# Kernel tuning notes

Hardware: AMD Instinct MI355X
Metric: run time of the kernel (lower is better)

## Reference

```python
import jax, jax.numpy as jnp
import numpy as np


def setup_inputs() -> dict:
    key = jax.random.key(0)
    k1, k2, k3, k4, k5 = jax.random.split(key, 5)
    B, S, D, F, E = 4, 4096, 1024, 2048, 8
    top_k = 2
    num_tokens = B * S
    capacity = max(int(num_tokens / E * 1.25), 4)  # 2560
    scale = 0.02
    return {
        "x": jax.random.normal(k1, (B, S, D), dtype=jnp.float32),
        "gate_w": jax.random.normal(k2, (D, E), dtype=jnp.float32) * scale,
        "w_gate": jax.random.normal(k3, (E, D, F), dtype=jnp.float32) * scale,
        "w_up": jax.random.normal(k4, (E, D, F), dtype=jnp.float32) * scale,
        "w_down": jax.random.normal(k5, (E, F, D), dtype=jnp.float32) * scale,
        "num_experts": E,
        "top_k": top_k,
        "capacity": capacity,
    }


AUX_LOSS_WEIGHT = 0.01


def reference(x, gate_w, w_gate, w_up, w_down, num_experts, top_k, capacity):
    B, S, D = x.shape
    N = B * S
    x_flat = x.reshape(N, D)

    # ---- Router ----
    logits = x_flat @ gate_w                      # [N, E]
    probs = jax.nn.softmax(logits, axis=-1)
    weights, indices = jax.lax.top_k(probs, top_k)  # [N, K]
    weights = weights / jnp.sum(weights, axis=-1, keepdims=True)

    # ---- Capacity-based dispatch ----
    indices_flat = indices.reshape(-1)            # [N*K]
    x_rep = jnp.repeat(x_flat, top_k, axis=0)     # [N*K, D]
    expert_mask = jax.nn.one_hot(indices_flat, num_experts, dtype=jnp.int32)  # [N*K, E]
    token_priority = jnp.cumsum(expert_mask, axis=0) * expert_mask
    token_rank = jnp.sum(token_priority, axis=1)  # [N*K], 1-based rank within expert
    valid = (token_rank > 0) & (token_rank <= capacity)
    gather_idx = indices_flat * capacity + (token_rank - 1)  # [N*K]

    total_slots = num_experts * capacity
    # drop-mode scatter: invalid rows are sent out-of-bounds and dropped
    safe_idx = jnp.where(valid, gather_idx, total_slots)
    dispatched = jnp.zeros((total_slots, D), dtype=x.dtype)
    dispatched = dispatched.at[safe_idx].set(x_rep, mode="drop")
    dispatched = dispatched.reshape(num_experts, capacity, D)  # [E, C, D]

    # ---- Fused experts (grouped BMM, SwiGLU) ----
    gate = jnp.einsum("ecd,edf->ecf", dispatched, w_gate)
    up = jnp.einsum("ecd,edf->ecf", dispatched, w_up)
    hidden = jax.nn.silu(gate) * up
    expert_out = jnp.einsum("ecf,efd->ecd", hidden, w_down)
    expert_out_flat = expert_out.reshape(total_slots, D)

    # ---- Combine (row-aligned gather; dropped tokens contribute zero) ----
    gathered = expert_out_flat[jnp.clip(gather_idx, 0, total_slots - 1)]
    combined = jnp.where(valid[:, None], gathered, jnp.zeros((), dtype=x.dtype))
    combined = combined.reshape(N, top_k, D)
    output = jnp.sum(combined * weights[:, :, None], axis=1)  # [N, D]

    # ---- Aux load-balance loss ----
    mask = jax.nn.one_hot(indices, num_experts, dtype=jnp.float32).sum(axis=1)  # [N, E]
    f = mask.sum(axis=0) / (N * top_k + 1e-9)
    P = probs.mean(axis=0)
    aux_loss = num_experts * jnp.sum(f * P) * AUX_LOSS_WEIGHT

    return output.reshape(B, S, D), aux_loss
```

## Files before the change

kernel.cpp:

```cpp
#include <hip/hip_runtime.h>
#include <stdint.h>

#define N_TOK 16384
#define DIM   1024
#define NEXP  8
#define FF    2048
#define CAP   2560
#define NSLOT (NEXP*CAP)

using f32x4  = __attribute__((ext_vector_type(4))) float;
using bf16x8 = __attribute__((ext_vector_type(8))) short;

__device__ __forceinline__ unsigned short f2bf(float f){
  union { float f; unsigned u; } c; c.f = f;
  unsigned u = c.u + 0x7FFFu + ((c.u >> 16) & 1u);
  return (unsigned short)(u >> 16);
}
__device__ __forceinline__ float bf2f(unsigned short h){
  union { unsigned u; float f; } c; c.u = ((unsigned)h) << 16; return c.f;
}

__device__ __forceinline__ void gld16(const unsigned short* g, unsigned short* l){
  __builtin_amdgcn_global_load_lds((__attribute__((address_space(1))) void*)(void*)g,
                                   (__attribute__((address_space(3))) void*)l,
                                   16, 0, 0);
}

#define HBAR __builtin_amdgcn_s_barrier()

__global__ __launch_bounds__(256) void k_router(
    const float* __restrict__ x, const float* __restrict__ gate_w,
    float* __restrict__ probs, int* __restrict__ topidx, float* __restrict__ topw)
{
  __shared__ float gwT[NEXP][DIM];
  int tid = threadIdx.x;
  for (int i = tid; i < DIM*NEXP; i += 256) gwT[i & 7][i >> 3] = gate_w[i];
  __syncthreads();
  int wave = tid >> 6, lane = tid & 63;
  int t = blockIdx.x * 4 + wave;
  const float* xr = x + (size_t)t * DIM;
  double acc[NEXP];
  #pragma unroll
  for (int e = 0; e < NEXP; e++) acc[e] = 0.0;
  for (int j = 0; j < DIM/64; j++){
    double xv = (double)xr[lane + 64*j];
    #pragma unroll
    for (int e = 0; e < NEXP; e++) acc[e] += xv * (double)gwT[e][lane + 64*j];
  }
  #pragma unroll
  for (int off = 32; off >= 1; off >>= 1){
    #pragma unroll
    for (int e = 0; e < NEXP; e++) acc[e] += __shfl_xor(acc[e], off, 64);
  }
  if (lane == 0){
    double m = acc[0];
    #pragma unroll
    for (int e = 1; e < NEXP; e++) m = fmax(m, acc[e]);
    double p[NEXP], Z = 0.0;
    #pragma unroll
    for (int e = 0; e < NEXP; e++){ p[e] = exp(acc[e] - m); Z += p[e]; }
    double invZ = 1.0 / Z;
    #pragma unroll
    for (int e = 0; e < NEXP; e++){ p[e] *= invZ; probs[t*NEXP + e] = (float)p[e]; }
    int i0 = 0; double p0 = p[0];
    #pragma unroll
    for (int e = 1; e < NEXP; e++) if (p[e] > p0){ p0 = p[e]; i0 = e; }
    int i1 = (i0 == 0) ? 1 : 0; double p1 = p[i1];
    #pragma unroll
    for (int e = 0; e < NEXP; e++) if (e != i0 && p[e] > p1){ p1 = p[e]; i1 = e; }
    double s = p0 + p1;
    topidx[t*2+0] = i0; topidx[t*2+1] = i1;
    topw [t*2+0] = (float)(p0/s); topw[t*2+1] = (float)(p1/s);
  }
}

__global__ __launch_bounds__(1024) void k_scan(
    const int* __restrict__ topidx,
    int* __restrict__ slot_token, int* __restrict__ tok_slots,
    int* __restrict__ counts_total)
{
  __shared__ int sc[1024][NEXP];
  const int t = threadIdx.x;
  const int base_i = t * 32;
  int ids[32];
  #pragma unroll
  for (int j = 0; j < 32; j++) ids[j] = topidx[base_i + j];
  int b[NEXP];
  #pragma unroll
  for (int e = 0; e < NEXP; e++) b[e] = 0;
  #pragma unroll
  for (int j = 0; j < 32; j++){
    #pragma unroll
    for (int e = 0; e < NEXP; e++) if (ids[j] == e) b[e]++;
  }
  #pragma unroll
  for (int e = 0; e < NEXP; e++) sc[t][e] = b[e];
  __syncthreads();
  for (int off = 1; off < 1024; off <<= 1){
    int tmp[NEXP];
    #pragma unroll
    for (int e = 0; e < NEXP; e++) tmp[e] = (t >= off) ? sc[t-off][e] : 0;
    __syncthreads();
    #pragma unroll
    for (int e = 0; e < NEXP; e++) sc[t][e] += tmp[e];
    __syncthreads();
  }
  int myb[NEXP];
  #pragma unroll
  for (int e = 0; e < NEXP; e++) myb[e] = sc[t][e] - b[e];
  if (t == 1023){
    #pragma unroll
    for (int e = 0; e < NEXP; e++) counts_total[e] = sc[1023][e];
  }
  #pragma unroll
  for (int j = 0; j < 32; j++){
    int slot = -1;
    #pragma unroll
    for (int e = 0; e < NEXP; e++){
      if (ids[j] == e){
        int r = myb[e]; myb[e] = r + 1;
        if (r < CAP){
          slot = e*CAP + r;
          slot_token[slot] = (base_i + j) >> 1;
        }
      }
    }
    tok_slots[base_i + j] = slot;
  }
}

template<int MODE>
__global__ __launch_bounds__(256) void k_tcv(
    const float* __restrict__ in, unsigned short* __restrict__ out,
    int R, int C, size_t estride)
{
  __shared__ float tt[64][65];
  const int e  = blockIdx.z;
  const float* ine = in + (size_t)e * R * C;
  unsigned short* oute = out + (size_t)e * estride;
  const int c0 = blockIdx.x * 64, r0 = blockIdx.y * 64;
  const int tid = threadIdx.x;
  #pragma unroll
  for (int i = 0; i < 4; i++){
    int idx = i*256 + tid;
    int row = idx >> 4, c4 = idx & 15;
    float4 v = *(const float4*)(ine + (size_t)(r0 + row)*C + c0 + c4*4);
    tt[c4*4+0][row] = v.x; tt[c4*4+1][row] = v.y;
    tt[c4*4+2][row] = v.z; tt[c4*4+3][row] = v.w;
  }
  __syncthreads();
  #pragma unroll
  for (int i = 0; i < 2; i++){
    int cl = i*32 + (tid >> 3);
    int rs = (tid & 7) * 8;
    int c  = c0 + cl;
    int orow = (MODE == 0) ? ((c>>4)*32 + (c&15))
             : (MODE == 1) ? ((c>>4)*32 + 16 + (c&15))
             : c;
    unsigned long long pk0 = 0, pk1 = 0;
    #pragma unroll
    for (int j = 0; j < 4; j++) pk0 |= (unsigned long long)f2bf(tt[cl][rs+j]) << (16*j);
    #pragma unroll
    for (int j = 0; j < 4; j++) pk1 |= (unsigned long long)f2bf(tt[cl][rs+4+j]) << (16*j);
    unsigned long long* dst = (unsigned long long*)(oute + (size_t)orow*R + r0 + rs);
    dst[0] = pk0; dst[1] = pk1;
  }
}

__global__ __launch_bounds__(256) void k_gather(
    const float* __restrict__ x, const int* __restrict__ slot_token,
    unsigned short* __restrict__ disp)
{
  const int s = blockIdx.x;
  const int t = slot_token[s];
  const int tid = threadIdx.x;
  unsigned long long pk = 0ull;
  if (t >= 0){
    float4 v = *(const float4*)(x + (size_t)t*DIM + tid*4);
    pk =  (unsigned long long)f2bf(v.x)
       | ((unsigned long long)f2bf(v.y) << 16)
       | ((unsigned long long)f2bf(v.z) << 32)
       | ((unsigned long long)f2bf(v.w) << 48);
  }
  *(unsigned long long*)(disp + (size_t)s*DIM + tid*4) = pk;
}

__device__ __forceinline__ void stg(const unsigned short* gsrc, int ldg,
                                    unsigned short* Lh, int wave, int lane){
  const int sl = (lane & 3) ^ ((lane >> 3) & 3);
  #pragma unroll
  for (int j = 0; j < 2; j++){
    int bi = wave*2 + j;
    gld16(gsrc + (size_t)(bi*16 + (lane >> 2))*ldg + sl*8, Lh + bi*512);
  }
}
__device__ __forceinline__ bf16x8 frd(const unsigned short* Lh, int r, int g){
  return *(const bf16x8*)(Lh + r*32 + (((g ^ ((r >> 1) & 3))) << 3));
}
template<int MG>
__device__ __forceinline__ void mm16(f32x4 (&acc)[8][4], const bf16x8 (&a)[4], const bf16x8 (&b)[4]){
  #pragma unroll
  for (int i = 0; i < 4; i++)
    #pragma unroll
    for (int n = 0; n < 4; n++)
      acc[MG*4+i][n] = __builtin_amdgcn_mfma_f32_16x16x32_bf16(a[i], b[n], acc[MG*4+i][n], 0, 0, 0);
}

__global__ __launch_bounds__(512, 2) void k_gemm1(
    const unsigned short* __restrict__ A,
    const unsigned short* __restrict__ B,
    unsigned short* __restrict__ Out)
{
  constexpr int KDIM = DIM, NH = DIM/32;
  __shared__ unsigned short lds[65536];
  const int id = blockIdx.x;
  const int e  = id & 7;
  const int t  = id >> 3;
  const int mt = t % 10, nt = t / 10;
  const int m0 = mt*256, n0 = nt*256;
  const unsigned short* Ab = A + ((size_t)e*CAP  + m0) * KDIM;
  const unsigned short* Bb = B + ((size_t)e*2*FF + n0) * KDIM;
  const int tid = threadIdx.x, wave = tid >> 6, lane = tid & 63;
  const int wr = wave >> 2, wc = wave & 3;
  const int g = lane >> 4, l15 = lane & 15;

  f32x4 acc[8][4];
  const f32x4 z4 = {0.f,0.f,0.f,0.f};
  #pragma unroll
  for (int i = 0; i < 8; i++)
    #pragma unroll
    for (int n = 0; n < 4; n++) acc[i][n] = z4;

  stg(Ab,      KDIM, lds + 0*16384,        wave, lane);
  stg(Bb,      KDIM, lds + 0*16384 + 8192, wave, lane);
  stg(Ab + 32, KDIM, lds + 1*16384,        wave, lane);
  stg(Bb + 32, KDIM, lds + 1*16384 + 8192, wave, lane);
  stg(Ab + 64, KDIM, lds + 2*16384,        wave, lane);
  stg(Bb + 64, KDIM, lds + 2*16384 + 8192, wave, lane);

  for (int h = 0; h < NH; ++h){
    if (h < NH-2)      { asm volatile("s_waitcnt vmcnt(8)" ::: "memory"); }
    else if (h == NH-2){ asm volatile("s_waitcnt vmcnt(4)" ::: "memory"); }
    else               { asm volatile("s_waitcnt vmcnt(0)" ::: "memory"); }
    HBAR;
    __builtin_amdgcn_sched_barrier(0);
    unsigned short* LA = lds + (h & 3)*16384;
    unsigned short* LB = LA + 8192;
    if (h + 3 < NH){
      unsigned short* NS = lds + ((h+3) & 3)*16384;
      stg(Ab + (size_t)(h+3)*32, KDIM, NS,        wave, lane);
      stg(Bb + (size_t)(h+3)*32, KDIM, NS + 8192, wave, lane);
    }
    bf16x8 a[4], b[4], a2[4];
    #pragma unroll
    for (int i = 0; i < 4; i++) a[i]  = frd(LA, wr*128 + i*16 + l15, g);
    #pragma unroll
    for (int n = 0; n < 4; n++) b[n]  = frd(LB, wc*64 + n*16 + l15, g);
    #pragma unroll
    for (int i = 0; i < 4; i++) a2[i] = frd(LA, wr*128 + (4+i)*16 + l15, g);
    __builtin_amdgcn_s_setprio(1);
    mm16<0>(acc, a, b);
    mm16<1>(acc, a2, b);
    __builtin_amdgcn_s_setprio(0);
  }

  unsigned short* H = Out + ((size_t)e*CAP + m0 + wr*128) * (size_t)FF;
  const int hc0 = (n0 + wc*64) >> 1;
  #pragma unroll
  for (int mf = 0; mf < 8; mf++)
    #pragma unroll
    for (int q = 0; q < 4; q++){
      int r = mf*16 + g*4 + q;
      #pragma unroll
      for (int p = 0; p < 2; p++){
        float gg = acc[mf][2*p][q], uu = acc[mf][2*p+1][q];
        float h = gg / (1.f + __expf(-gg)) * uu;
        H[(size_t)r*FF + hc0 + p*16 + l15] = f2bf(h);
      }
    }
}

__global__ __launch_bounds__(256, 2) void k_gemm2s(
    const unsigned short* __restrict__ A,
    const unsigned short* __restrict__ B,
    unsigned short* __restrict__ Out)
{
  constexpr int KDIM = FF, NH = FF/32;
  __shared__ unsigned short lds[32768];
  const int id = blockIdx.x;
  const int e  = id & 7;
  const int t  = id >> 3;
  const int mt = t % 20, nt = t / 20;
  const int m0 = mt*128, n0 = nt*128;
  const unsigned short* Ab = A + ((size_t)e*CAP + m0) * KDIM;
  const unsigned short* Bb = B + ((size_t)e*DIM + n0) * KDIM;
  const int tid = threadIdx.x, wave = tid >> 6, lane = tid & 63;
  const int wr = wave >> 1, wc = wave & 1;
  const int g = lane >> 4, l15 = lane & 15;

  f32x4 acc[4][4];
  const f32x4 z4 = {0.f,0.f,0.f,0.f};
  #pragma unroll
  for (int i = 0; i < 4; i++)
    #pragma unroll
    for (int n = 0; n < 4; n++) acc[i][n] = z4;

  stg(Ab,      KDIM, lds + 0*8192,        wave, lane);
  stg(Bb,      KDIM, lds + 0*8192 + 4096, wave, lane);
  stg(Ab + 32, KDIM, lds + 1*8192,        wave, lane);
  stg(Bb + 32, KDIM, lds + 1*8192 + 4096, wave, lane);
  stg(Ab + 64, KDIM, lds + 2*8192,        wave, lane);
  stg(Bb + 64, KDIM, lds + 2*8192 + 4096, wave, lane);

  for (int h = 0; h < NH; ++h){
    if (h < NH-2)      { asm volatile("s_waitcnt vmcnt(8)" ::: "memory"); }
    else if (h == NH-2){ asm volatile("s_waitcnt vmcnt(4)" ::: "memory"); }
    else               { asm volatile("s_waitcnt vmcnt(0)" ::: "memory"); }
    HBAR;
    __builtin_amdgcn_sched_barrier(0);
    unsigned short* LA = lds + (h & 3)*8192;
    unsigned short* LB = LA + 4096;
    if (h + 3 < NH){
      unsigned short* NS = lds + ((h+3) & 3)*8192;
      stg(Ab + (size_t)(h+3)*32, KDIM, NS,        wave, lane);
      stg(Bb + (size_t)(h+3)*32, KDIM, NS + 4096, wave, lane);
    }
    bf16x8 a[4], b[4];
    #pragma unroll
    for (int i = 0; i < 4; i++) a[i] = frd(LA, wr*64 + i*16 + l15, g);
    #pragma unroll
    for (int n = 0; n < 4; n++) b[n] = frd(LB, wc*64 + n*16 + l15, g);
    __builtin_amdgcn_s_setprio(1);
    #pragma unroll
    for (int i = 0; i < 4; i++)
      #pragma unroll
      for (int n = 0; n < 4; n++)
        acc[i][n] = __builtin_amdgcn_mfma_f32_16x16x32_bf16(a[i], b[n], acc[i][n], 0, 0, 0);
    __builtin_amdgcn_s_setprio(0);
  }

  unsigned short* O = Out + ((size_t)e*CAP + m0 + wr*64) * (size_t)DIM + n0 + wc*64;
  #pragma unroll
  for (int mf = 0; mf < 4; mf++)
    #pragma unroll
    for (int q = 0; q < 4; q++){
      int r = mf*16 + g*4 + q;
      #pragma unroll
      for (int n = 0; n < 4; n++)
        O[(size_t)r*DIM + n*16 + l15] = f2bf(acc[mf][n][q]);
    }
}

__global__ __launch_bounds__(256) void k_combine(
    const unsigned short* __restrict__ slot_out, const int* __restrict__ tok_slots,
    const float* __restrict__ topw, float* __restrict__ out)
{
  const int t = blockIdx.x*2 + (threadIdx.x >> 7);
  const int tid = threadIdx.x & 127;
  const int s0 = tok_slots[t*2+0], s1 = tok_slots[t*2+1];
  const float w0 = topw[t*2+0], w1 = topw[t*2+1];
  float r[8];
  #pragma unroll
  for (int j = 0; j < 8; j++) r[j] = 0.f;
  if (s0 >= 0){
    bf16x8 v = *(const bf16x8*)(slot_out + (size_t)s0*DIM + tid*8);
    #pragma unroll
    for (int j = 0; j < 8; j++) r[j] += w0 * bf2f((unsigned short)v[j]);
  }
  if (s1 >= 0){
    bf16x8 v = *(const bf16x8*)(slot_out + (size_t)s1*DIM + tid*8);
    #pragma unroll
    for (int j = 0; j < 8; j++) r[j] += w1 * bf2f((unsigned short)v[j]);
  }
  float4* o = (float4*)(out + (size_t)t*DIM + tid*8);
  o[0] = make_float4(r[0], r[1], r[2], r[3]);
  o[1] = make_float4(r[4], r[5], r[6], r[7]);
}

__global__ __launch_bounds__(256) void k_aux(
    const float* __restrict__ probs, const int* __restrict__ counts_total,
    float* __restrict__ aux_out)
{
  const int tid = threadIdx.x;
  float pe[NEXP];
  #pragma unroll
  for (int e = 0; e < NEXP; e++) pe[e] = 0.f;
  for (int i = tid; i < N_TOK; i += 256){
    #pragma unroll
    for (int e = 0; e < NEXP; e++) pe[e] += probs[i*NEXP + e];
  }
  #pragma unroll
  for (int off = 32; off >= 1; off >>= 1){
    #pragma unroll
    for (int e = 0; e < NEXP; e++) pe[e] += __shfl_xor(pe[e], off, 64);
  }
  __shared__ float part[4][NEXP];
  const int wave = tid >> 6, lane = tid & 63;
  if (lane == 0){
    #pragma unroll
    for (int e = 0; e < NEXP; e++) part[wave][e] = pe[e];
  }
  __syncthreads();
  if (tid == 0){
    float aux = 0.f;
    for (int e = 0; e < NEXP; e++){
      float P = (part[0][e] + part[1][e] + part[2][e] + part[3][e]) / (float)N_TOK;
      float f = (float)counts_total[e] / ((float)(N_TOK*2) + 1e-9f);
      aux += f * P;
    }
    aux_out[0] = (float)NEXP * aux * 0.01f;
  }
}

extern "C" void kernel_launch(void* const* d_in, const int* in_sizes, int n_in,
                              void* d_out, int out_size, void* d_ws, size_t ws_size,
                              hipStream_t stream)
{
  const float* x      = (const float*)d_in[0];
  const float* gate_w = (const float*)d_in[1];
  const float* w_gate = (const float*)d_in[2];
  const float* w_up   = (const float*)d_in[3];
  const float* w_down = (const float*)d_in[4];
  float* out = (float*)d_out;

  uint8_t* ws = (uint8_t*)d_ws;
  float* probs        = (float*)ws;             ws += (size_t)N_TOK*NEXP*4;
  int*   topidx       = (int*)ws;               ws += (size_t)N_TOK*2*4;
  float* topw         = (float*)ws;             ws += (size_t)N_TOK*2*4;
  int*   slot_token   = (int*)ws;               ws += (size_t)NSLOT*4;
  int*   tok_slots    = (int*)ws;               ws += (size_t)N_TOK*2*4;
  int*   counts_total = (int*)ws;               ws += 256;
  unsigned short* disp   = (unsigned short*)ws; ws += (size_t)NSLOT*DIM*2;
  unsigned short* hidden = (unsigned short*)ws; ws += (size_t)NSLOT*FF*2;
  unsigned short* B1     = (unsigned short*)ws; ws += (size_t)NEXP*2*FF*DIM*2;
  unsigned short* wdT    = (unsigned short*)ws; ws += (size_t)NEXP*DIM*FF*2;
  size_t need = (size_t)(ws - (uint8_t*)d_ws);
  if (ws_size < need) return;
  unsigned short* slot_out = disp;

  hipMemsetAsync(slot_token, 0xFF, (size_t)NSLOT * sizeof(int), stream);

  k_router<<<N_TOK/4, 256, 0, stream>>>(x, gate_w, probs, topidx, topw);
  k_scan<<<1, 1024, 0, stream>>>(topidx, slot_token, tok_slots, counts_total);
  k_tcv<0><<<dim3(FF/64, DIM/64, NEXP), 256, 0, stream>>>(w_gate, B1, DIM, FF, (size_t)2*FF*DIM);
  k_tcv<1><<<dim3(FF/64, DIM/64, NEXP), 256, 0, stream>>>(w_up,   B1, DIM, FF, (size_t)2*FF*DIM);
  k_tcv<2><<<dim3(DIM/64, FF/64, NEXP), 256, 0, stream>>>(w_down, wdT, FF, DIM, (size_t)DIM*FF);
  k_gather<<<NSLOT, 256, 0, stream>>>(x, slot_token, disp);
  k_gemm1<<<1280, 512, 0, stream>>>(disp, B1, hidden);
  k_gemm2s<<<1280, 256, 0, stream>>>(hidden, wdT, slot_out);
  k_combine<<<N_TOK/2, 256, 0, stream>>>(slot_out, tok_slots, topw, out);
  k_aux<<<1, 256, 0, stream>>>(probs, counts_total, out + (size_t)N_TOK*DIM);
}
```

Measured before the change: 520.2 us.

## Prefetch next K-step LDS fragments into registers before MFMA in expert GEMMs

Both expert GEMM kernels now read the A/B fragments for the next K-step from LDS into registers before running the current step's MFMAs, so LDS read latency overlaps with matrix math. The vmcnt waits are tightened by one stage to match, and the loop is unrolled by 4. In exchange it raises register pressure from the extra fragment buffers, and the shallower global-load wait slack may expose memory latency.

```diff
diff --git a/kernel.cpp b/kernel.cpp
--- a/kernel.cpp
+++ b/kernel.cpp
@@ -27,6 +27,7 @@
 }
 
 #define HBAR __builtin_amdgcn_s_barrier()
+#define SBAR0 __builtin_amdgcn_sched_barrier(0)
 
 __global__ __launch_bounds__(256) void k_router(
     const float* __restrict__ x, const float* __restrict__ gate_w,
@@ -237,31 +238,43 @@
   stg(Bb + 32, KDIM, lds + 1*16384 + 8192, wave, lane);
   stg(Ab + 64, KDIM, lds + 2*16384,        wave, lane);
   stg(Bb + 64, KDIM, lds + 2*16384 + 8192, wave, lane);
-
+  asm volatile("s_waitcnt vmcnt(8)" ::: "memory");
+  HBAR;
+  bf16x8 ca[4], cb[4];
+  #pragma unroll
+  for (int i = 0; i < 4; i++) ca[i] = frd(lds,        wr*128 + i*16 + l15, g);
+  #pragma unroll
+  for (int n = 0; n < 4; n++) cb[n] = frd(lds + 8192, wc*64  + n*16 + l15, g);
+
+  #pragma unroll 4
   for (int h = 0; h < NH; ++h){
-    if (h < NH-2)      { asm volatile("s_waitcnt vmcnt(8)" ::: "memory"); }
-    else if (h == NH-2){ asm volatile("s_waitcnt vmcnt(4)" ::: "memory"); }
-    else               { asm volatile("s_waitcnt vmcnt(0)" ::: "memory"); }
+    if (h < NH-2)      { asm volatile("s_waitcnt vmcnt(4)" ::: "memory"); }
+    else if (h == NH-2){ asm volatile("s_waitcnt vmcnt(0)" ::: "memory"); }
     HBAR;
-    __builtin_amdgcn_sched_barrier(0);
-    unsigned short* LA = lds + (h & 3)*16384;
-    unsigned short* LB = LA + 8192;
+    bf16x8 na[4], nb[4];
+    if (h + 1 < NH){
+      unsigned short* NL = lds + ((h+1) & 3)*16384;
+      #pragma unroll
+      for (int i = 0; i < 4; i++) na[i] = frd(NL,        wr*128 + i*16 + l15, g);
+      #pragma unroll
+      for (int n = 0; n < 4; n++) nb[n] = frd(NL + 8192, wc*64  + n*16 + l15, g);
+    }
     if (h + 3 < NH){
       unsigned short* NS = lds + ((h+3) & 3)*16384;
       stg(Ab + (size_t)(h+3)*32, KDIM, NS,        wave, lane);
       stg(Bb + (size_t)(h+3)*32, KDIM, NS + 8192, wave, lane);
     }
-    bf16x8 a[4], b[4], a2[4];
-    #pragma unroll
-    for (int i = 0; i < 4; i++) a[i]  = frd(LA, wr*128 + i*16 + l15, g);
-    #pragma unroll
-    for (int n = 0; n < 4; n++) b[n]  = frd(LB, wc*64 + n*16 + l15, g);
+    SBAR0;
+    unsigned short* LA = lds + (h & 3)*16384;
+    bf16x8 a2[4];
     #pragma unroll
     for (int i = 0; i < 4; i++) a2[i] = frd(LA, wr*128 + (4+i)*16 + l15, g);
     __builtin_amdgcn_s_setprio(1);
-    mm16<0>(acc, a, b);
-    mm16<1>(acc, a2, b);
+    mm16<0>(acc, ca, cb);
+    mm16<1>(acc, a2, cb);
     __builtin_amdgcn_s_setprio(0);
+    #pragma unroll
+    for (int i = 0; i < 4; i++){ ca[i] = na[i]; cb[i] = nb[i]; }
   }
 
   unsigned short* H = Out + ((size_t)e*CAP + m0 + wr*128) * (size_t)FF;
@@ -311,32 +324,42 @@
   stg(Bb + 32, KDIM, lds + 1*8192 + 4096, wave, lane);
   stg(Ab + 64, KDIM, lds + 2*8192,        wave, lane);
   stg(Bb + 64, KDIM, lds + 2*8192 + 4096, wave, lane);
-
+  asm volatile("s_waitcnt vmcnt(8)" ::: "memory");
+  HBAR;
+  bf16x8 ca[4], cb[4];
+  #pragma unroll
+  for (int i = 0; i < 4; i++) ca[i] = frd(lds,        wr*64 + i*16 + l15, g);
+  #pragma unroll
+  for (int n = 0; n < 4; n++) cb[n] = frd(lds + 4096, wc*64 + n*16 + l15, g);
+
+  #pragma unroll 4
   for (int h = 0; h < NH; ++h){
-    if (h < NH-2)      { asm volatile("s_waitcnt vmcnt(8)" ::: "memory"); }
-    else if (h == NH-2){ asm volatile("s_waitcnt vmcnt(4)" ::: "memory"); }
-    else               { asm volatile("s_waitcnt vmcnt(0)" ::: "memory"); }
+    if (h < NH-2)      { asm volatile("s_waitcnt vmcnt(4)" ::: "memory"); }
+    else if (h == NH-2){ asm volatile("s_waitcnt vmcnt(0)" ::: "memory"); }
     HBAR;
-    __builtin_amdgcn_sched_barrier(0);
-    unsigned short* LA = lds + (h & 3)*8192;
-    unsigned short* LB = LA + 4096;
+    bf16x8 na[4], nb[4];
+    if (h + 1 < NH){
+      unsigned short* NL = lds + ((h+1) & 3)*8192;
+      #pragma unroll
+      for (int i = 0; i < 4; i++) na[i] = frd(NL,        wr*64 + i*16 + l15, g);
+      #pragma unroll
+      for (int n = 0; n < 4; n++) nb[n] = frd(NL + 4096, wc*64 + n*16 + l15, g);
+    }
     if (h + 3 < NH){
       unsigned short* NS = lds + ((h+3) & 3)*8192;
       stg(Ab + (size_t)(h+3)*32, KDIM, NS,        wave, lane);
       stg(Bb + (size_t)(h+3)*32, KDIM, NS + 4096, wave, lane);
     }
-    bf16x8 a[4], b[4];
-    #pragma unroll
-    for (int i = 0; i < 4; i++) a[i] = frd(LA, wr*64 + i*16 + l15, g);
-    #pragma unroll
-    for (int n = 0; n < 4; n++) b[n] = frd(LB, wc*64 + n*16 + l15, g);
+    SBAR0;
     __builtin_amdgcn_s_setprio(1);
     #pragma unroll
     for (int i = 0; i < 4; i++)
       #pragma unroll
       for (int n = 0; n < 4; n++)
-        acc[i][n] = __builtin_amdgcn_mfma_f32_16x16x32_bf16(a[i], b[n], acc[i][n], 0, 0, 0);
+        acc[i][n] = __builtin_amdgcn_mfma_f32_16x16x32_bf16(ca[i], cb[n], acc[i][n], 0, 0, 0);
     __builtin_amdgcn_s_setprio(0);
+    #pragma unroll
+    for (int i = 0; i < 4; i++){ ca[i] = na[i]; cb[i] = nb[i]; }
   }
 
   unsigned short* O = Out + ((size_t)e*CAP + m0 + wr*64) * (size_t)DIM + n0 + wc*64;
```

After: 787.9 us. 1.51x slower.
